# Kernel optimization log

Measured on AMD Instinct MI355X. Metric: run time of the kernel, lower is better.

The kernel has to match this reference:

```python
import jax, jax.numpy as jnp
import numpy as np

N = 50000   # nodes
E = 800000  # edges (avg degree 16)
NEG = 0.2   # leaky_relu negative slope


def gat_conv(feat, W, al, ar, rW, src, dst, act):
    """DGL-style GATConv. feat:[N,F] W:[F,H*D] al/ar:[H,D] rW:[F,H*D] or None (identity residual)."""
    n = feat.shape[0]
    H, D = al.shape
    h = (feat @ W).reshape(n, H, D)                      # [N,H,D]
    el = jnp.einsum('nhd,hd->nh', h, al)                 # [N,H]
    er = jnp.einsum('nhd,hd->nh', h, ar)                 # [N,H]
    e = el[src] + er[dst]                                # [E,H]
    e = jnp.where(e > 0, e, NEG * e)                     # leaky_relu
    emax = jax.ops.segment_max(e, dst, num_segments=n)   # per-dst softmax (edge softmax)
    ee = jnp.exp(e - emax[dst])
    denom = jax.ops.segment_sum(ee, dst, num_segments=n)
    alpha = ee / denom[dst]                              # [E,H]
    out = jax.ops.segment_sum(h[src] * alpha[:, :, None], dst, num_segments=n)  # [N,H,D]
    res = (feat @ rW).reshape(n, H, D) if rW is not None else feat.reshape(n, H, D)
    return act(out + res)


def setup_inputs() -> dict:
    key = jax.random.key(0)
    ks = jax.random.split(key, 32)
    d = {}
    d["fvs"] = jax.random.normal(ks[0], (N, 128), jnp.float32)
    d["pos_enc"] = jax.random.normal(ks[1], (N, 64), jnp.float32)
    d["src"] = jax.random.randint(ks[2], (E,), 0, N, jnp.int32)
    d["dst"] = jax.random.randint(ks[3], (E,), 0, N, jnp.int32)
    def w(k, shape):
        return jax.random.normal(k, shape, jnp.float32) / np.sqrt(shape[0])
    i = 4
    # gat layers: in=192 -> H=2, D=64 (layers 0,1), final: H=2, D=64 (out_ch)
    for name in ["gat0", "gat1", "gat2"]:
        d[name + "_W"] = w(ks[i], (192, 128)); i += 1
        d[name + "_al"] = w(ks[i], (2, 64)); i += 1
        d[name + "_ar"] = w(ks[i], (2, 64)); i += 1
        d[name + "_rW"] = w(ks[i], (192, 128)); i += 1
    # pgnn layers: in=64 -> H=2, D=32; in == H*D so residual is identity (no rW)
    for name in ["pg0", "pg1"]:
        d[name + "_W"] = w(ks[i], (64, 64)); i += 1
        d[name + "_al"] = w(ks[i], (2, 32)); i += 1
        d[name + "_ar"] = w(ks[i], (2, 32)); i += 1
    return d


def reference(fvs, pos_enc, src, dst,
              gat0_W, gat0_al, gat0_ar, gat0_rW,
              gat1_W, gat1_al, gat1_ar, gat1_rW,
              gat2_W, gat2_al, gat2_ar, gat2_rW,
              pg0_W, pg0_al, pg0_ar,
              pg1_W, pg1_al, pg1_ar):
    n = fvs.shape[0]
    h_s, h_p = fvs, pos_enc
    # layer 0
    h_s = jnp.concatenate([h_s, h_p], axis=1)
    h_s = gat_conv(h_s, gat0_W, gat0_al, gat0_ar, gat0_rW, src, dst, jax.nn.elu).reshape(n, -1)
    h_p = gat_conv(h_p, pg0_W, pg0_al, pg0_ar, None, src, dst, jnp.tanh).reshape(n, -1)
    # layer 1
    h_s = jnp.concatenate([h_s, h_p], axis=1)
    h_s = gat_conv(h_s, gat1_W, gat1_al, gat1_ar, gat1_rW, src, dst, jax.nn.elu).reshape(n, -1)
    h_p = gat_conv(h_p, pg1_W, pg1_al, pg1_ar, None, src, dst, jnp.tanh).reshape(n, -1)
    # output layer: mean over heads
    h_s = jnp.concatenate([h_s, h_p], axis=1)
    h_s = gat_conv(h_s, gat2_W, gat2_al, gat2_ar, gat2_rW, src, dst, jax.nn.elu).mean(axis=1)
    return (h_s, h_p)
```

## Files before the change

### kernel.cpp

```cpp
#include <hip/hip_runtime.h>

#define NN 50000
#define NE 800000

typedef unsigned short u16;
typedef unsigned int u32;

typedef float f32x4 __attribute__((ext_vector_type(4)));
typedef __bf16 bf16x8 __attribute__((ext_vector_type(8)));
static_assert(sizeof(bf16x8) == 16, "bf16x8 must be 16B");

__device__ __forceinline__ float bf2f(u16 u) {
    u32 x = ((u32)u) << 16;
    return __uint_as_float(x);
}
__device__ __forceinline__ u16 f2bf(float f) {
    u32 x = __float_as_uint(f);
    u32 r = (x + 0x7fffu + ((x >> 16) & 1u)) >> 16;
    return (u16)r;
}
__device__ __forceinline__ u32 pack2(float a, float b) {
    return (u32)f2bf(a) | ((u32)f2bf(b) << 16);
}
__device__ __forceinline__ u16 f2h(float f) {
    _Float16 h = (_Float16)f;
    union { _Float16 h; u16 u; } c; c.h = h;
    return c.u;
}
__device__ __forceinline__ float h2f(u16 u) {
    union { u16 u; _Float16 h; } c; c.u = u;
    return (float)c.h;
}
__device__ __forceinline__ uint4 packu4(const u16* h) {
    uint4 u;
    u.x = (u32)h[0] | ((u32)h[1] << 16);
    u.y = (u32)h[2] | ((u32)h[3] << 16);
    u.z = (u32)h[4] | ((u32)h[5] << 16);
    u.w = (u32)h[6] | ((u32)h[7] << 16);
    return u;
}
__device__ __forceinline__ float ldf(const void* p, size_t idx, int mode) {
    return mode ? bf2f(((const u16*)p)[idx]) : ((const float*)p)[idx];
}
__device__ __forceinline__ float lrelu(float x) { return x > 0.f ? x : 0.2f * x; }

__device__ __forceinline__ f32x4 mfma16(uint4 a, uint4 b, f32x4 c) {
    union { uint4 u; bf16x8 b; } ua, ub;
    ua.u = a; ub.u = b;
    return __builtin_amdgcn_mfma_f32_16x16x32_bf16(ua.b, ub.b, c, 0, 0, 0);
}

__global__ void k_tracer(float* out, float v) {
    if (threadIdx.x == 0 && blockIdx.x == 0) out[0] = v;
}

__global__ void k_detect(const u16* __restrict__ fvs, int* __restrict__ mode) {
    __shared__ int cnt[256];
    int t = threadIdx.x;
    int bad = 0;
    for (int i = 0; i < 16; i++) {
        u16 u = fvs[(size_t)(t * 16 + i) * 2];
        int e = (u >> 7) & 0xff;
        if (e == 255 || e >= 134 || e <= 100) bad++;
    }
    cnt[t] = bad;
    __syncthreads();
    for (int d = 128; d; d >>= 1) {
        if (t < d) cnt[t] += cnt[t + d];
        __syncthreads();
    }
    if (t == 0) *mode = (cnt[0] > 2048) ? 0 : 1;
}

__global__ void k_hist(const int* __restrict__ dst, int* __restrict__ cnt, int E) {
    int e = blockIdx.x * blockDim.x + threadIdx.x;
    if (e < E) atomicAdd(&cnt[dst[e]], 1);
}

__global__ void k_scan1(const int* __restrict__ cnt, int* __restrict__ off,
                        int* __restrict__ bsum, int N) {
    __shared__ int wsum[4];
    int t = threadIdx.x;
    int base = blockIdx.x * 2048 + t * 8;
    int e[8];
    if (base + 8 <= N) {
        int4 v0 = *(const int4*)&cnt[base];
        int4 v1 = *(const int4*)&cnt[base + 4];
        e[0] = v0.x; e[1] = v0.y; e[2] = v0.z; e[3] = v0.w;
        e[4] = v1.x; e[5] = v1.y; e[6] = v1.z; e[7] = v1.w;
    } else {
#pragma unroll
        for (int i = 0; i < 8; i++) e[i] = (base + i < N) ? cnt[base + i] : 0;
    }
    int s = 0;
    int ps[8];
#pragma unroll
    for (int i = 0; i < 8; i++) { ps[i] = s; s += e[i]; }
    int lane = t & 63, wv = t >> 6;
    int sc = s;
#pragma unroll
    for (int o = 1; o < 64; o <<= 1) {
        int u = __shfl_up(sc, o, 64);
        if (lane >= o) sc += u;
    }
    if (lane == 63) wsum[wv] = sc;
    __syncthreads();
    int woff = 0;
    for (int w = 0; w < wv; w++) woff += wsum[w];
    int ex = woff + sc - s;
#pragma unroll
    for (int i = 0; i < 8; i++) ps[i] += ex;
    if (base + 8 <= N) {
        *(int4*)&off[base] = make_int4(ps[0], ps[1], ps[2], ps[3]);
        *(int4*)&off[base + 4] = make_int4(ps[4], ps[5], ps[6], ps[7]);
    } else {
#pragma unroll
        for (int i = 0; i < 8; i++)
            if (base + i < N) off[base + i] = ps[i];
    }
    if (t == 255) bsum[blockIdx.x] = woff + sc;
}

__global__ void k_scan2(const int* __restrict__ bsum, int* __restrict__ off,
                        int N, int nb) {
    int b = blockIdx.x, t = threadIdx.x;
    int boff = 0;
    for (int i = 0; i < b; i++) boff += bsum[i];
    int base = b * 2048 + t * 8;
    if (b > 0) {
        if (base + 8 <= N) {
            int4 a = *(int4*)&off[base];
            int4 c = *(int4*)&off[base + 4];
            a.x += boff; a.y += boff; a.z += boff; a.w += boff;
            c.x += boff; c.y += boff; c.z += boff; c.w += boff;
            *(int4*)&off[base] = a;
            *(int4*)&off[base + 4] = c;
        } else {
#pragma unroll
            for (int i = 0; i < 8; i++)
                if (base + i < N) off[base + i] += boff;
        }
    }
    if (b == nb - 1 && t == 255) off[N] = boff + bsum[b];
}

__global__ void k_fill(const int* __restrict__ src, const int* __restrict__ dst,
                       const int* __restrict__ off, int* __restrict__ cnt2,
                       int* __restrict__ ssrc, int E) {
    int e = blockIdx.x * blockDim.x + threadIdx.x;
    if (e < E) {
        int d = dst[e];
        int p = off[d] + atomicAdd(&cnt2[d], 1);
        ssrc[p] = src[e];
    }
}

__global__ void k_init(const void* __restrict__ pos, u16* __restrict__ hp,
                       const int* __restrict__ dmode, int n64) {
    int i = blockIdx.x * blockDim.x + threadIdx.x;
    if (i >= n64) return;
    int mode = *dmode;
    hp[i] = mode ? ((const u16*)pos)[i] : f2bf(((const float*)pos)[i]);
}

__global__ void k_cvt(const u16* __restrict__ in, float* __restrict__ out, int n) {
    int i = blockIdx.x * blockDim.x + threadIdx.x;
    if (i < n) out[i] = bf2f(in[i]);
}

struct PWArgs {
    const void* src[8];
    u16* dst[8];
    int K[8];
    int BM[8];
};

__global__ void k_prepw(PWArgs a, const int* __restrict__ dmode) {
    int mode = *dmode;
    int g = blockIdx.x * blockDim.x + threadIdx.x;
    int stride = gridDim.x * blockDim.x;
    for (int m = 0; m < 8; m++) {
        int bm = a.BM[m];
        int bmsh = (bm == 128) ? 7 : 6;
        int n = a.K[m] * bm;
        u16* d = a.dst[m];
        const void* s = a.src[m];
        for (int i = g; i < n; i += stride) {
            int k = i >> bmsh, c = i & (bm - 1);
            float v = mode ? bf2f(((const u16*)s)[i]) : ((const float*)s)[i];
            u16 hi = f2bf(v);
            u16 lo = f2bf(v - bf2f(hi));
            size_t o = ((size_t)((k >> 5) * 2) * bm + c) * 32 + (k & 31);
            d[o] = hi;
            d[o + (size_t)bm * 32] = lo;
        }
    }
}

template <int BM, bool HASB2, bool C1H>
__launch_bounds__(256, 3)
__global__ void k_gemm(const void* A1, const u16* __restrict__ A2,
                       const u16* __restrict__ B1p, const u16* __restrict__ B2p,
                       void* __restrict__ C1, u16* C2, float* __restrict__ att,
                       const void* __restrict__ al, const void* __restrict__ ar,
                       int N, int K, int s1, const int* __restrict__ dmode,
                       int a1_input) {
    constexpr int NR = BM / 32;
    constexpr int NMAT = HASB2 ? 2 : 1;

    __shared__ u16 As[2][64][40];

    const int mode = *dmode;
    const int a1f32 = (a1_input && mode == 0) ? 1 : 0;
    const int bsplit = (mode == 0) ? 1 : 0;

    const int tid = threadIdx.x;
    const int lane = tid & 63;
    const int wid = tid >> 6;
    const int l15 = lane & 15, l4 = lane >> 4;
    const int r0 = blockIdx.x * 64;
    const int wrow0 = (wid >> 1) * 32;
    const int wcol0 = (wid & 1) * (BM / 2);

    const int arow = tid >> 2;
    const int akh = (tid & 3) * 8;
    const int gra = r0 + arow;

    uint4 pa[2] = {};
    auto loadA = [&](int k0) {
        if (gra >= N) return;
        if (k0 >= 128) {
            pa[0] = *(const uint4*)(A2 + (size_t)gra * 64 + (k0 - 128) + akh);
        } else if (!a1f32) {
            pa[0] = *(const uint4*)((const u16*)A1 + (size_t)gra * s1 + k0 + akh);
        } else {
            const float* p = (const float*)A1 + (size_t)gra * s1 + k0 + akh;
            pa[0] = *(const uint4*)p;
            pa[1] = *(const uint4*)(p + 4);
        }
    };

    auto stageA = [&](int k0, int asplit) {
        const int abf = (k0 >= 128 || !a1f32);
        if (abf) {
            uint4 z = {0, 0, 0, 0};
            *(uint4*)&As[0][arow][akh] = (gra < N) ? pa[0] : z;
        } else {
            const float* f = (const float*)pa;
            u16 hi[8], lo[8];
#pragma unroll
            for (int i = 0; i < 8; i++) {
                float v = (gra < N) ? f[i] : 0.f;
                hi[i] = f2bf(v);
                lo[i] = f2bf(v - bf2f(hi[i]));
            }
            *(uint4*)&As[0][arow][akh] = packu4(hi);
            if (asplit) *(uint4*)&As[1][arow][akh] = packu4(lo);
        }
    };

    f32x4 acc[NMAT][2][NR];
    const f32x4 fz = {0.f, 0.f, 0.f, 0.f};
#pragma unroll
    for (int m2 = 0; m2 < NMAT; m2++)
#pragma unroll
        for (int m = 0; m < 2; m++)
#pragma unroll
            for (int n = 0; n < NR; n++) acc[m2][m][n] = fz;

    loadA(0);
    const int NKT = K >> 5;
    for (int kt = 0; kt < NKT; kt++) {
        const int k0 = kt << 5;
        const int doAlo = (a1f32 && k0 < 128) ? 1 : 0;
        __syncthreads();
        stageA(k0, doAlo);
        __syncthreads();
        if (kt + 1 < NKT) loadA(k0 + 32);

        uint4 ah[2], alo[2];
#pragma unroll
        for (int m = 0; m < 2; m++)
            ah[m] = *(const uint4*)&As[0][wrow0 + m * 16 + l15][l4 * 8];
        if (doAlo) {
#pragma unroll
            for (int m = 0; m < 2; m++)
                alo[m] = *(const uint4*)&As[1][wrow0 + m * 16 + l15][l4 * 8];
        }

        const size_t bbase = ((size_t)kt * 2) * BM * 32 + (size_t)l4 * 8;
#pragma unroll
        for (int n = 0; n < NR; n++) {
            const int c = wcol0 + n * 16 + l15;
            const size_t co = (size_t)c * 32;
#pragma unroll
            for (int m2 = 0; m2 < NMAT; m2++) {
                const u16* bp = (m2 == 0 ? B1p : B2p) + bbase + co;
                uint4 bh = *(const uint4*)bp;
#pragma unroll
                for (int m = 0; m < 2; m++)
                    acc[m2][m][n] = mfma16(ah[m], bh, acc[m2][m][n]);
                if (bsplit) {
                    uint4 bl = *(const uint4*)(bp + (size_t)BM * 32);
#pragma unroll
                    for (int m = 0; m < 2; m++)
                        acc[m2][m][n] = mfma16(ah[m], bl, acc[m2][m][n]);
                }
                if (doAlo) {
#pragma unroll
                    for (int m = 0; m < 2; m++)
                        acc[m2][m][n] = mfma16(alo[m], bh, acc[m2][m][n]);
                }
            }
        }
    }

    float alc[NR], arc[NR];
#pragma unroll
    for (int n = 0; n < NR; n++) {
        int c = wcol0 + n * 16 + l15;
        alc[n] = ldf(al, c, mode);
        arc[n] = ldf(ar, c, mode);
    }
    const int hc = wid & 1;
#pragma unroll
    for (int m = 0; m < 2; m++) {
#pragma unroll
        for (int r = 0; r < 4; r++) {
            const int gr = r0 + wrow0 + m * 16 + l4 * 4 + r;
            float el = 0.f, er = 0.f;
#pragma unroll
            for (int n = 0; n < NR; n++) {
                float v = acc[0][m][n][r];
                el = fmaf(v, alc[n], el);
                er = fmaf(v, arc[n], er);
            }
#pragma unroll
            for (int o = 1; o <= 8; o <<= 1) {
                el += __shfl_xor(el, o, 64);
                er += __shfl_xor(er, o, 64);
            }
            if (gr < N) {
#pragma unroll
                for (int n = 0; n < NR; n++) {
                    const int c = wcol0 + n * 16 + l15;
                    float v = acc[0][m][n][r];
                    if constexpr (C1H)
                        ((u16*)C1)[(size_t)gr * BM + c] = f2h(v);
                    else
                        ((float*)C1)[(size_t)gr * BM + c] = v;
                    if constexpr (HASB2)
                        C2[(size_t)gr * 128 + c] = f2bf(acc[1][m][n][r]);
                }
                if (l15 == 0) {
                    att[(size_t)gr * 4 + hc] = el;
                    att[(size_t)gr * 4 + 2 + hc] = er;
                }
            }
        }
    }
}

__global__ void k_edge_gat2(const int* __restrict__ off, const int* __restrict__ ssrc,
                            const u16* __restrict__ h, const float* __restrict__ att,
                            const u16* __restrict__ res, u16* __restrict__ outf, int N) {
    __shared__ float pbuf[4][2][64];
    __shared__ int sbuf[4][64];
    int wv = threadIdx.x >> 6;
    int node = blockIdx.x * 4 + wv;
    int lane = threadIdx.x & 63;
    if (node >= N) return;
    const int hd = lane >> 5;
    int beg = off[node], end = off[node + 1];
    float4 a4 = *(const float4*)&att[(size_t)node * 4];
    float er0 = a4.z, er1 = a4.w;
    float m0 = -1e30f, m1 = -1e30f, d0 = 0.f, d1 = 0.f, O0 = 0.f, O1 = 0.f;
    for (int c = beg; c < end; c += 64) {
        int cn = min(end - c, 64);
        int s = 0;
        float x0 = -1e30f, x1 = -1e30f;
        if (lane < cn) {
            s = ssrc[c + lane];
            float2 e = *(const float2*)&att[(size_t)s * 4];
            x0 = lrelu(e.x + er0);
            x1 = lrelu(e.y + er1);
        }
        float cm0 = x0, cm1 = x1;
#pragma unroll
        for (int o = 32; o; o >>= 1) {
            cm0 = fmaxf(cm0, __shfl_xor(cm0, o, 64));
            cm1 = fmaxf(cm1, __shfl_xor(cm1, o, 64));
        }
        float nm0 = fmaxf(m0, cm0), nm1 = fmaxf(m1, cm1);
        float p0 = (lane < cn) ? __expf(x0 - nm0) : 0.f;
        float p1 = (lane < cn) ? __expf(x1 - nm1) : 0.f;
        float cd0 = p0, cd1 = p1;
#pragma unroll
        for (int o = 32; o; o >>= 1) {
            cd0 += __shfl_xor(cd0, o, 64);
            cd1 += __shfl_xor(cd1, o, 64);
        }
        float sc0 = __expf(m0 - nm0), sc1 = __expf(m1 - nm1);
        d0 = d0 * sc0 + cd0; d1 = d1 * sc1 + cd1;
        float sch = hd ? sc1 : sc0;
        O0 *= sch; O1 *= sch;
        m0 = nm0; m1 = nm1;
        pbuf[wv][0][lane] = p0;
        pbuf[wv][1][lane] = p1;
        sbuf[wv][lane] = s;
        const float* pb = pbuf[wv][hd];
        int j = 0;
        for (; j + 3 < cn; j += 4) {
            int s0 = sbuf[wv][j], s1 = sbuf[wv][j + 1];
            int s2 = sbuf[wv][j + 2], s3 = sbuf[wv][j + 3];
            u32 w0 = *(const u32*)&h[(size_t)s0 * 128 + 2 * lane];
            u32 w1 = *(const u32*)&h[(size_t)s1 * 128 + 2 * lane];
            u32 w2 = *(const u32*)&h[(size_t)s2 * 128 + 2 * lane];
            u32 w3 = *(const u32*)&h[(size_t)s3 * 128 + 2 * lane];
            float q0 = pb[j], q1 = pb[j + 1], q2 = pb[j + 2], q3 = pb[j + 3];
            O0 += q0 * h2f((u16)w0) + q1 * h2f((u16)w1)
                + q2 * h2f((u16)w2) + q3 * h2f((u16)w3);
            O1 += q0 * h2f((u16)(w0 >> 16)) + q1 * h2f((u16)(w1 >> 16))
                + q2 * h2f((u16)(w2 >> 16)) + q3 * h2f((u16)(w3 >> 16));
        }
        for (; j < cn; j++) {
            u32 w = *(const u32*)&h[(size_t)sbuf[wv][j] * 128 + 2 * lane];
            float q = pb[j];
            O0 += q * h2f((u16)w);
            O1 += q * h2f((u16)(w >> 16));
        }
    }
    float dd = hd ? d1 : d0;
    float o0 = (end > beg) ? O0 / dd : 0.f;
    float o1 = (end > beg) ? O1 / dd : 0.f;
    u32 rv = *(const u32*)&res[(size_t)node * 128 + 2 * lane];
    float a0 = o0 + bf2f((u16)rv);
    float a1 = o1 + bf2f((u16)(rv >> 16));
    a0 = a0 > 0.f ? a0 : (__expf(a0) - 1.f);
    a1 = a1 > 0.f ? a1 : (__expf(a1) - 1.f);
    *(u32*)&outf[(size_t)node * 128 + 2 * lane] = pack2(a0, a1);
}

__global__ void k_edge_gat_f(const int* __restrict__ off, const int* __restrict__ ssrc,
                             const u16* __restrict__ h, const float* __restrict__ att,
                             const u16* __restrict__ res, float* __restrict__ outs, int N) {
    __shared__ float pbuf[4][2][64];
    __shared__ int sbuf[4][64];
    int wv = threadIdx.x >> 6;
    int node = blockIdx.x * 4 + wv;
    int lane = threadIdx.x & 63;
    if (node >= N) return;
    const int par = lane >> 5;
    const int i = lane & 31;
    const int hd = i >> 4;
    int beg = off[node], end = off[node + 1];
    float4 a4 = *(const float4*)&att[(size_t)node * 4];
    float er0 = a4.z, er1 = a4.w;
    float m0 = -1e30f, m1 = -1e30f, d0 = 0.f, d1 = 0.f;
    float O[4] = {0.f, 0.f, 0.f, 0.f};
    for (int c = beg; c < end; c += 64) {
        int cn = min(end - c, 64);
        int s = 0;
        float x0 = -1e30f, x1 = -1e30f;
        if (lane < cn) {
            s = ssrc[c + lane];
            float2 e = *(const float2*)&att[(size_t)s * 4];
            x0 = lrelu(e.x + er0);
            x1 = lrelu(e.y + er1);
        }
        float cm0 = x0, cm1 = x1;
#pragma unroll
        for (int o = 32; o; o >>= 1) {
            cm0 = fmaxf(cm0, __shfl_xor(cm0, o, 64));
            cm1 = fmaxf(cm1, __shfl_xor(cm1, o, 64));
        }
        float nm0 = fmaxf(m0, cm0), nm1 = fmaxf(m1, cm1);
        float p0 = (lane < cn) ? __expf(x0 - nm0) : 0.f;
        float p1 = (lane < cn) ? __expf(x1 - nm1) : 0.f;
        float cd0 = p0, cd1 = p1;
#pragma unroll
        for (int o = 32; o; o >>= 1) {
            cd0 += __shfl_xor(cd0, o, 64);
            cd1 += __shfl_xor(cd1, o, 64);
        }
        float sc0 = __expf(m0 - nm0), sc1 = __expf(m1 - nm1);
        d0 = d0 * sc0 + cd0; d1 = d1 * sc1 + cd1;
        float sch = hd ? sc1 : sc0;
#pragma unroll
        for (int k = 0; k < 4; k++) O[k] *= sch;
        m0 = nm0; m1 = nm1;
        pbuf[wv][0][lane] = p0;
        pbuf[wv][1][lane] = p1;
        sbuf[wv][lane] = s;
        const float* pb = pbuf[wv][hd];
        int j = par;
        for (; j + 6 < cn; j += 8) {
            int s0 = sbuf[wv][j], s1 = sbuf[wv][j + 2];
            int s2 = sbuf[wv][j + 4], s3 = sbuf[wv][j + 6];
            uint2 w0 = *(const uint2*)&h[(size_t)s0 * 128 + 4 * i];
            uint2 w1 = *(const uint2*)&h[(size_t)s1 * 128 + 4 * i];
            uint2 w2 = *(const uint2*)&h[(size_t)s2 * 128 + 4 * i];
            uint2 w3 = *(const uint2*)&h[(size_t)s3 * 128 + 4 * i];
            float q0 = pb[j], q1 = pb[j + 2], q2 = pb[j + 4], q3 = pb[j + 6];
            O[0] += q0 * h2f((u16)w0.x) + q1 * h2f((u16)w1.x)
                  + q2 * h2f((u16)w2.x) + q3 * h2f((u16)w3.x);
            O[1] += q0 * h2f((u16)(w0.x >> 16)) + q1 * h2f((u16)(w1.x >> 16))
                  + q2 * h2f((u16)(w2.x >> 16)) + q3 * h2f((u16)(w3.x >> 16));
            O[2] += q0 * h2f((u16)w0.y) + q1 * h2f((u16)w1.y)
                  + q2 * h2f((u16)w2.y) + q3 * h2f((u16)w3.y);
            O[3] += q0 * h2f((u16)(w0.y >> 16)) + q1 * h2f((u16)(w1.y >> 16))
                  + q2 * h2f((u16)(w2.y >> 16)) + q3 * h2f((u16)(w3.y >> 16));
        }
        for (; j < cn; j += 2) {
            uint2 w = *(const uint2*)&h[(size_t)sbuf[wv][j] * 128 + 4 * i];
            float q = pb[j];
            O[0] += q * h2f((u16)w.x);
            O[1] += q * h2f((u16)(w.x >> 16));
            O[2] += q * h2f((u16)w.y);
            O[3] += q * h2f((u16)(w.y >> 16));
        }
    }
#pragma unroll
    for (int k = 0; k < 4; k++) O[k] += __shfl_xor(O[k], 32, 64);
    float dd = hd ? d1 : d0;
    uint2 rv = *(const uint2*)&res[(size_t)node * 128 + 4 * i];
    float a[4];
    a[0] = bf2f((u16)rv.x);
    a[1] = bf2f((u16)(rv.x >> 16));
    a[2] = bf2f((u16)rv.y);
    a[3] = bf2f((u16)(rv.y >> 16));
#pragma unroll
    for (int k = 0; k < 4; k++) {
        float o = (end > beg) ? O[k] / dd : 0.f;
        float v = o + a[k];
        a[k] = v > 0.f ? v : (__expf(v) - 1.f);
    }
    float b[4];
#pragma unroll
    for (int k = 0; k < 4; k++) b[k] = __shfl_xor(a[k], 16, 64);
    if (lane < 16)
        *(float4*)&outs[(size_t)node * 64 + 4 * i] =
            make_float4(0.5f * (a[0] + b[0]), 0.5f * (a[1] + b[1]),
                        0.5f * (a[2] + b[2]), 0.5f * (a[3] + b[3]));
}

__global__ void k_edge_pg2(const int* __restrict__ off, const int* __restrict__ ssrc,
                           const u16* __restrict__ h, const float* __restrict__ att,
                           u16* __restrict__ hp, int N) {
    __shared__ float pbuf[4][2][64];
    __shared__ int sbuf[4][64];
    int wv = threadIdx.x >> 6;
    int node = blockIdx.x * 4 + wv;
    int lane = threadIdx.x & 63;
    if (node >= N) return;
    const int par = lane >> 5;
    const int i = lane & 31;
    const int hd = i >> 4;
    int beg = off[node], end = off[node + 1];
    float4 a4 = *(const float4*)&att[(size_t)node * 4];
    float er0 = a4.z, er1 = a4.w;
    float m0 = -1e30f, m1 = -1e30f, d0 = 0.f, d1 = 0.f, O0 = 0.f, O1 = 0.f;
    for (int c = beg; c < end; c += 64) {
        int cn = min(end - c, 64);
        int s = 0;
        float x0 = -1e30f, x1 = -1e30f;
        if (lane < cn) {
            s = ssrc[c + lane];
            float2 e = *(const float2*)&att[(size_t)s * 4];
            x0 = lrelu(e.x + er0);
            x1 = lrelu(e.y + er1);
        }
        float cm0 = x0, cm1 = x1;
#pragma unroll
        for (int o = 32; o; o >>= 1) {
            cm0 = fmaxf(cm0, __shfl_xor(cm0, o, 64));
            cm1 = fmaxf(cm1, __shfl_xor(cm1, o, 64));
        }
        float nm0 = fmaxf(m0, cm0), nm1 = fmaxf(m1, cm1);
        float p0 = (lane < cn) ? __expf(x0 - nm0) : 0.f;
        float p1 = (lane < cn) ? __expf(x1 - nm1) : 0.f;
        float cd0 = p0, cd1 = p1;
#pragma unroll
        for (int o = 32; o; o >>= 1) {
            cd0 += __shfl_xor(cd0, o, 64);
            cd1 += __shfl_xor(cd1, o, 64);
        }
        float sc0 = __expf(m0 - nm0), sc1 = __expf(m1 - nm1);
        d0 = d0 * sc0 + cd0; d1 = d1 * sc1 + cd1;
        float sch = hd ? sc1 : sc0;
        O0 *= sch; O1 *= sch;
        m0 = nm0; m1 = nm1;
        pbuf[wv][0][lane] = p0;
        pbuf[wv][1][lane] = p1;
        sbuf[wv][lane] = s;
        const float* pb = pbuf[wv][hd];
        int j = par;
        for (; j + 6 < cn; j += 8) {
            int s0 = sbuf[wv][j], s1 = sbuf[wv][j + 2];
            int s2 = sbuf[wv][j + 4], s3 = sbuf[wv][j + 6];
            u32 w0 = *(const u32*)&h[(size_t)s0 * 64 + 2 * i];
            u32 w1 = *(const u32*)&h[(size_t)s1 * 64 + 2 * i];
            u32 w2 = *(const u32*)&h[(size_t)s2 * 64 + 2 * i];
            u32 w3 = *(const u32*)&h[(size_t)s3 * 64 + 2 * i];
            float q0 = pb[j], q1 = pb[j + 2], q2 = pb[j + 4], q3 = pb[j + 6];
            O0 += q0 * h2f((u16)w0) + q1 * h2f((u16)w1)
                + q2 * h2f((u16)w2) + q3 * h2f((u16)w3);
            O1 += q0 * h2f((u16)(w0 >> 16)) + q1 * h2f((u16)(w1 >> 16))
                + q2 * h2f((u16)(w2 >> 16)) + q3 * h2f((u16)(w3 >> 16));
        }
        for (; j < cn; j += 2) {
            u32 w = *(const u32*)&h[(size_t)sbuf[wv][j] * 64 + 2 * i];
            float q = pb[j];
            O0 += q * h2f((u16)w);
            O1 += q * h2f((u16)(w >> 16));
        }
    }
    O0 += __shfl_xor(O0, 32, 64);
    O1 += __shfl_xor(O1, 32, 64);
    if (lane < 32) {
        float dd = hd ? d1 : d0;
        float o0 = (end > beg) ? O0 / dd : 0.f;
        float o1 = (end > beg) ? O1 / dd : 0.f;
        u32 rv = *(const u32*)&hp[(size_t)node * 64 + 2 * i];
        float a0 = tanhf(o0 + bf2f((u16)rv));
        float a1 = tanhf(o1 + bf2f((u16)(rv >> 16)));
        *(u32*)&hp[(size_t)node * 64 + 2 * i] = pack2(a0, a1);
    }
}

extern "C" void kernel_launch(void* const* d_in, const int* in_sizes, int n_in,
                              void* d_out, int out_size, void* d_ws, size_t ws_size,
                              hipStream_t stream) {
    const int N = NN, E = NE;
    const void* fvs = d_in[0];
    const void* pos = d_in[1];
    const int* src = (const int*)d_in[2];
    const int* dst = (const int*)d_in[3];
    const void* gW[3]  = {d_in[4],  d_in[8],  d_in[12]};
    const void* gal[3] = {d_in[5],  d_in[9],  d_in[13]};
    const void* gar[3] = {d_in[6],  d_in[10], d_in[14]};
    const void* grW[3] = {d_in[7],  d_in[11], d_in[15]};
    const void* pW[2]  = {d_in[16], d_in[19]};
    const void* pal[2] = {d_in[17], d_in[20]};
    const void* par[2] = {d_in[18], d_in[21]};

    auto al256 = [](size_t b) { return (b + 255) & ~(size_t)255; };
    size_t sz_dmode = al256(4);
    size_t sz_bsum  = al256(32 * 4);
    size_t sz_att   = al256((size_t)N * 4 * 4);
    size_t sz_off   = al256((size_t)(N + 1) * 4);
    size_t sz_ssrc  = al256((size_t)E * 4);
    size_t sz_hs    = al256((size_t)N * 128 * 2);
    size_t sz_hp    = al256((size_t)N * 64 * 2);
    size_t sz_wpk   = al256((size_t)(6 * 192 * 128 + 2 * 64 * 64) * 2 * 2);
    size_t need = sz_dmode + sz_bsum + sz_att + sz_off + sz_ssrc + sz_hs + sz_hp + sz_wpk;
    int bad = (need > ws_size) ? 1 : 0;

    size_t cur = 0;
    auto alloc = [&](size_t bytes) {
        if (cur + bytes > ws_size) cur = 0;
        char* p = (char*)d_ws + cur;
        if (bytes <= ws_size) cur += bytes;
        return p;
    };
    int* dmode  = (int*)alloc(sz_dmode);
    int* bsum   = (int*)alloc(sz_bsum);
    float* att  = (float*)alloc(sz_att);
    int* off    = (int*)alloc(sz_off);
    int* ssrc   = (int*)alloc(sz_ssrc);
    u16* hs     = (u16*)alloc(sz_hs);
    u16* hp     = (u16*)alloc(sz_hp);
    u16* wpk    = (u16*)alloc(sz_wpk);

    const size_t GSZ = (size_t)192 * 128 * 2;
    const size_t PSZ = (size_t)64 * 64 * 2;
    u16* Bp[8];
    for (int m = 0; m < 6; m++) Bp[m] = wpk + (size_t)m * GSZ;
    Bp[6] = wpk + 6 * GSZ;
    Bp[7] = Bp[6] + PSZ;

    int* cnt  = (int*)att;
    int* cnt2 = (int*)((char*)att + al256((size_t)N * 4));

    void* H = d_out;

    hipMemsetAsync(cnt, 0, (size_t)N * 4, stream);
    hipMemsetAsync(cnt2, 0, (size_t)N * 4, stream);

    k_detect<<<1, 256, 0, stream>>>((const u16*)fvs, dmode);

    PWArgs pwa;
    pwa.src[0] = gW[0]; pwa.src[1] = grW[0];
    pwa.src[2] = gW[1]; pwa.src[3] = grW[1];
    pwa.src[4] = gW[2]; pwa.src[5] = grW[2];
    pwa.src[6] = pW[0]; pwa.src[7] = pW[1];
    for (int m = 0; m < 8; m++) {
        pwa.dst[m] = Bp[m];
        pwa.K[m] = (m < 6) ? 192 : 64;
        pwa.BM[m] = (m < 6) ? 128 : 64;
    }
    k_prepw<<<64, 256, 0, stream>>>(pwa, dmode);

    int eb = (E + 255) / 256;
    int nbS = (N + 2047) / 2048;
    k_hist<<<eb, 256, 0, stream>>>(dst, cnt, E);
    k_scan1<<<nbS, 256, 0, stream>>>(cnt, off, bsum, N);
    k_scan2<<<nbS, 256, 0, stream>>>(bsum, off, N, nbS);
    k_fill<<<eb, 256, 0, stream>>>(src, dst, off, cnt2, ssrc, E);

    k_init<<<(N * 64 + 255) / 256, 256, 0, stream>>>(pos, hp, dmode, N * 64);

    int gb = (N + 63) / 64;
    int nb = (N + 3) / 4;

    k_gemm<128, true, true><<<gb, 256, 0, stream>>>(fvs, hp, Bp[0], Bp[1], H, hs, att, gal[0], gar[0], N, 192, 128, dmode, 1);
    k_edge_gat2<<<nb, 256, 0, stream>>>(off, ssrc, (u16*)H, att, hs, hs, N);
    k_gemm<64, false, true><<<gb, 256, 0, stream>>>(hp, nullptr, Bp[6], nullptr, H, nullptr, att, pal[0], par[0], N, 64, 64, dmode, 0);
    k_edge_pg2<<<nb, 256, 0, stream>>>(off, ssrc, (u16*)H, att, hp, N);

    k_gemm<128, true, true><<<gb, 256, 0, stream>>>(hs, hp, Bp[2], Bp[3], H, hs, att, gal[1], gar[1], N, 192, 128, dmode, 0);
    k_edge_gat2<<<nb, 256, 0, stream>>>(off, ssrc, (u16*)H, att, hs, hs, N);
    k_gemm<64, false, true><<<gb, 256, 0, stream>>>(hp, nullptr, Bp[7], nullptr, H, nullptr, att, pal[1], par[1], N, 64, 64, dmode, 0);
    k_edge_pg2<<<nb, 256, 0, stream>>>(off, ssrc, (u16*)H, att, hp, N);

    k_gemm<128, true, true><<<gb, 256, 0, stream>>>(hs, hp, Bp[4], Bp[5], H, hs, att, gal[2], gar[2], N, 192, 128, dmode, 0);
    k_edge_gat_f<<<nb, 256, 0, stream>>>(off, ssrc, (u16*)H, att, hs, (float*)hs, N);

    hipMemcpyAsync((float*)d_out, (float*)hs, (size_t)N * 64 * 4, hipMemcpyDeviceToDevice, stream);
    k_cvt<<<(N * 64 + 255) / 256, 256, 0, stream>>>(hp, (float*)d_out + (size_t)N * 64, N * 64);

    if (bad) {
        float v = 100000.f + 1000.f * (float)(ws_size >> 20);
        k_tracer<<<1, 64, 0, stream>>>((float*)d_out, v);
    }
}
```

Before: 587.2 us.

## Load GEMM A fragments directly from global memory, dropping LDS staging

Removes the shared-memory staging buffer for the A operand in the projection GEMM. Each lane now loads its MFMA A fragment straight from global memory, clamping out-of-range rows, and does any fp32 hi/lo split in registers. This drops two block barriers per k-tile, and occupancy is raised to 4 blocks per CU. In exchange, A rows are reloaded redundantly by the two column-split waves, the loads are no longer prefetched one tile ahead, and the per-wave access pattern may be less coalesced.

```diff
diff --git a/kernel.cpp b/kernel.cpp
--- a/kernel.cpp
+++ b/kernel.cpp
@@ -198,7 +198,7 @@
 }
 
 template <int BM, bool HASB2, bool C1H>
-__launch_bounds__(256, 3)
+__launch_bounds__(256, 4)
 __global__ void k_gemm(const void* A1, const u16* __restrict__ A2,
                        const u16* __restrict__ B1p, const u16* __restrict__ B2p,
                        void* __restrict__ C1, u16* C2, float* __restrict__ att,
@@ -208,8 +208,6 @@
     constexpr int NR = BM / 32;
     constexpr int NMAT = HASB2 ? 2 : 1;
 
-    __shared__ u16 As[2][64][40];
-
     const int mode = *dmode;
     const int a1f32 = (a1_input && mode == 0) ? 1 : 0;
     const int bsplit = (mode == 0) ? 1 : 0;
@@ -221,43 +219,14 @@
     const int r0 = blockIdx.x * 64;
     const int wrow0 = (wid >> 1) * 32;
     const int wcol0 = (wid & 1) * (BM / 2);
-
-    const int arow = tid >> 2;
-    const int akh = (tid & 3) * 8;
-    const int gra = r0 + arow;
-
-    uint4 pa[2] = {};
-    auto loadA = [&](int k0) {
-        if (gra >= N) return;
-        if (k0 >= 128) {
-            pa[0] = *(const uint4*)(A2 + (size_t)gra * 64 + (k0 - 128) + akh);
-        } else if (!a1f32) {
-            pa[0] = *(const uint4*)((const u16*)A1 + (size_t)gra * s1 + k0 + akh);
-        } else {
-            const float* p = (const float*)A1 + (size_t)gra * s1 + k0 + akh;
-            pa[0] = *(const uint4*)p;
-            pa[1] = *(const uint4*)(p + 4);
-        }
-    };
-
-    auto stageA = [&](int k0, int asplit) {
-        const int abf = (k0 >= 128 || !a1f32);
-        if (abf) {
-            uint4 z = {0, 0, 0, 0};
-            *(uint4*)&As[0][arow][akh] = (gra < N) ? pa[0] : z;
-        } else {
-            const float* f = (const float*)pa;
-            u16 hi[8], lo[8];
-#pragma unroll
-            for (int i = 0; i < 8; i++) {
-                float v = (gra < N) ? f[i] : 0.f;
-                hi[i] = f2bf(v);
-                lo[i] = f2bf(v - bf2f(hi[i]));
-            }
-            *(uint4*)&As[0][arow][akh] = packu4(hi);
-            if (asplit) *(uint4*)&As[1][arow][akh] = packu4(lo);
-        }
-    };
+    const int ko = l4 * 8;
+
+    int frow[2];
+#pragma unroll
+    for (int m = 0; m < 2; m++) {
+        int r = r0 + wrow0 + m * 16 + l15;
+        frow[m] = r < N ? r : N - 1;
+    }
 
     f32x4 acc[NMAT][2][NR];
     const f32x4 fz = {0.f, 0.f, 0.f, 0.f};
@@ -268,24 +237,32 @@
 #pragma unroll
             for (int n = 0; n < NR; n++) acc[m2][m][n] = fz;
 
-    loadA(0);
     const int NKT = K >> 5;
     for (int kt = 0; kt < NKT; kt++) {
         const int k0 = kt << 5;
         const int doAlo = (a1f32 && k0 < 128) ? 1 : 0;
-        __syncthreads();
-        stageA(k0, doAlo);
-        __syncthreads();
-        if (kt + 1 < NKT) loadA(k0 + 32);
 
         uint4 ah[2], alo[2];
 #pragma unroll
-        for (int m = 0; m < 2; m++)
-            ah[m] = *(const uint4*)&As[0][wrow0 + m * 16 + l15][l4 * 8];
-        if (doAlo) {
-#pragma unroll
-            for (int m = 0; m < 2; m++)
-                alo[m] = *(const uint4*)&As[1][wrow0 + m * 16 + l15][l4 * 8];
+        for (int m = 0; m < 2; m++) {
+            if (k0 >= 128) {
+                ah[m] = *(const uint4*)(A2 + (size_t)frow[m] * 64 + (k0 - 128) + ko);
+            } else if (!a1f32) {
+                ah[m] = *(const uint4*)((const u16*)A1 + (size_t)frow[m] * s1 + k0 + ko);
+            } else {
+                const float* p = (const float*)A1 + (size_t)frow[m] * s1 + k0 + ko;
+                union { uint4 u[2]; float f[8]; } fa;
+                fa.u[0] = *(const uint4*)p;
+                fa.u[1] = *(const uint4*)(p + 4);
+                u16 hi[8], lo[8];
+#pragma unroll
+                for (int i = 0; i < 8; i++) {
+                    hi[i] = f2bf(fa.f[i]);
+                    lo[i] = f2bf(fa.f[i] - bf2f(hi[i]));
+                }
+                ah[m] = packu4(hi);
+                alo[m] = packu4(lo);
+            }
         }
 
         const size_t bbase = ((size_t)kt * 2) * BM * 32 + (size_t)l4 * 8;
@@ -314,6 +291,8 @@
             }
         }
     }
+
+    __syncthreads();
 
     float alc[NR], arc[NR];
 #pragma unroll
```

Measured after the change: 574.7 us. -2.1%, faster.
